# Kernel optimization log

Measured on AMD Instinct MI355X. Metric: run time of the kernel, lower is better.

The kernel has to match this reference:

```python
import jax, jax.numpy as jnp
import numpy as np

TEMPERATURE = 0.07
EPS = 1e-8  # torch cosine_similarity clamps the norm product at eps


def setup_inputs() -> dict:
    key = jax.random.key(0)
    k1, k2 = jax.random.split(key)
    B, D = 8192, 256
    u = jax.random.normal(k1, (B, D), dtype=jnp.float32)
    v = jax.random.normal(k2, (B, D), dtype=jnp.float32)
    return {"u": u, "v": v}


def _cos_sim_matrix(a, b):
    # pairwise cosine similarity: (a . b) / max(|a||b|, eps)
    dots = a @ b.T                                   # [B, B]
    an = jnp.linalg.norm(a, axis=-1)                 # [B]
    bn = jnp.linalg.norm(b, axis=-1)                 # [B]
    denom = jnp.maximum(an[:, None] * bn[None, :], EPS)
    return dots / denom


def reference(u, v):
    B = u.shape[0]
    sim_uv = _cos_sim_matrix(u, v) / TEMPERATURE     # [B, B]
    sim_uu = _cos_sim_matrix(u, u) / TEMPERATURE     # [B, B]
    eye = jnp.eye(B, dtype=bool)
    pos_loss = jnp.diagonal(sim_uv)                  # [B]
    neg_inf = jnp.array(-jnp.inf, dtype=sim_uv.dtype)
    # off-diagonal entries of both matrices, concatenated per row (2B-2 valid each)
    negative_sim = jnp.concatenate(
        [jnp.where(eye, neg_inf, sim_uv), jnp.where(eye, neg_inf, sim_uu)], axis=1
    )                                                # [B, 2B]
    neg_loss = jax.nn.logsumexp(negative_sim, axis=-1)  # [B]
    return (-pos_loss + neg_loss).mean()
```

## Files before the change

kernel.cpp:

```cpp
#include <hip/hip_runtime.h>
#include <hip/hip_bf16.h>
#include <stdint.h>

#define NB 8192
#define ND 256
#define NW 16384
#define BM 128
#define BN 64
#define NSTRIP 4
#define STRIPW 4096
#define NPANEL (STRIPW / BN)
#define SQRT_SCALE 4.53981596f
#define LN2F 0.69314718f

typedef __bf16 bf16x8 __attribute__((ext_vector_type(8)));
typedef float floatx4 __attribute__((ext_vector_type(4)));

__device__ __forceinline__ void gload_lds16(const void* g, void* l) {
    __builtin_amdgcn_global_load_lds(
        (const __attribute__((address_space(1))) unsigned int*)g,
        (__attribute__((address_space(3))) unsigned int*)l,
        16, 0, 0);
}

__device__ __forceinline__ float fexp2(float x) {
    return __builtin_amdgcn_exp2f(x);
}

__global__ __launch_bounds__(512) void prep_kernel(
    const float* __restrict__ u, const float* __restrict__ v,
    __hip_bfloat16* __restrict__ W, float* __restrict__ out)
{
    const int t    = threadIdx.x;
    if (blockIdx.x == 0 && t == 0) out[0] = 0.f;
    const int row  = blockIdx.x * 8 + (t >> 6);
    const int lane = t & 63;
    const float* src = (row < NB) ? (v + (size_t)row * ND)
                                  : (u + (size_t)(row - NB) * ND);
    float4 x = ((const float4*)src)[lane];
    float ss = x.x * x.x + x.y * x.y + x.z * x.z + x.w * x.w;
#pragma unroll
    for (int off = 1; off < 64; off <<= 1) ss += __shfl_xor(ss, off, 64);
    const float sc = rsqrtf(ss) * SQRT_SCALE;
    ushort4 o;
    __hip_bfloat16 h;
    h = __float2bfloat16(x.x * sc); o.x = *(const unsigned short*)&h;
    h = __float2bfloat16(x.y * sc); o.y = *(const unsigned short*)&h;
    h = __float2bfloat16(x.z * sc); o.z = *(const unsigned short*)&h;
    h = __float2bfloat16(x.w * sc); o.w = *(const unsigned short*)&h;
    ((ushort4*)(W + (size_t)row * ND))[lane] = o;
}

__global__ __launch_bounds__(512, 2) void dcl_main(
    const __hip_bfloat16* __restrict__ W,
    float* __restrict__ partial,
    float* __restrict__ pos)
{
    const int b  = blockIdx.x;
    const int s  = (b >> 1) & 3;
    const int rt = ((b >> 3) << 1) | (b & 1);
    const int rb = rt * BM;

    const __hip_bfloat16* A = W + (size_t)NB * ND;

    __shared__ __align__(16) char lds[131072];

    const int tid  = threadIdx.x;
    const int wave = tid >> 6;
    const int lane = tid & 63;
    const int wm   = wave >> 2;
    const int wn   = wave & 3;
    const int quad = lane >> 4;
    const int tcol = lane & 15;
    const int rh   = lane >> 5;
    const int cl   = lane & 31;

    const int sbase = s * STRIPW;

#define WAITV(N) do {                                                        \
    asm volatile("s_waitcnt vmcnt(" #N ")" ::: "memory");                    \
    __builtin_amdgcn_sched_barrier(0);                                       \
} while (0)

#define STAGE(T) do {                                                        \
    char* dst_ = lds + ((T) & 3) * 32768 + wave * 4096;                      \
    const int cb_ = sbase + (T) * BN;                                        \
    _Pragma("unroll")                                                        \
    for (int i_ = 0; i_ < 4; i_++) {                                         \
        int rl_ = wave * 8 + i_ * 2 + rh;               \
        gload_lds16(W + (size_t)(cb_ + rl_) * ND + ((cl ^ (rl_ & 15)) << 3), \
                    dst_ + i_ * 1024);                                       \
    }                                                                        \
} while (0)

#define COMPUTE(T) do {                                                      \
    const char* sb_ = lds + ((T) & 3) * 32768;                               \
    _Pragma("unroll")                                                        \
    for (int mt_ = 0; mt_ < 4; mt_++) acc[mt_] = (floatx4){0.f,0.f,0.f,0.f}; \
    _Pragma("unroll")                                                        \
    for (int ks_ = 0; ks_ < 8; ks_++) {                                      \
        bf16x8 bb_ = *(const bf16x8*)(sb_ + (wn * 16 + tcol) * 512 +         \
                                      ((((ks_ * 4) + quad) ^ tcol) << 4));   \
        _Pragma("unroll")                                                    \
        for (int mt_ = 0; mt_ < 4; mt_++)                                    \
            acc[mt_] = __builtin_amdgcn_mfma_f32_16x16x32_bf16(              \
                af[mt_][ks_], bb_, acc[mt_], 0, 0, 0);                       \
    }                                                                        \
} while (0)

#define EPILOGUE(T) do {                                                     \
    const int cbE_ = sbase + (T) * BN;                                       \
    if (cbE_ != dp) {                                                        \
        _Pragma("unroll")                                                    \
        for (int mt_ = 0; mt_ < 4; mt_++)                                    \
            _Pragma("unroll")                                                \
            for (int rg_ = 0; rg_ < 4; rg_++)                                \
                rsum[mt_][rg_] += fexp2(acc[mt_][rg_]);                      \
    } else {                                                                 \
        _Pragma("unroll")                                                    \
        for (int mt_ = 0; mt_ < 4; mt_++)                                    \
            _Pragma("unroll")                                                \
            for (int rg_ = 0; rg_ < 4; rg_++) {                              \
                int rl_ = mt_ * 16 + quad * 4 + rg_;                         \
                bool sel_ = (rl_ == wn * 16 + tcol);                         \
                float sc_ = acc[mt_][rg_];                                   \
                if (sel_) posv = sc_;                                        \
                rsum[mt_][rg_] += sel_ ? 0.f : fexp2(sc_);                   \
            }                                                                \
    }                                                                        \
} while (0)

#define PANEL_BODY(T) do {                                                   \
    __builtin_amdgcn_s_setprio(1);                                           \
    COMPUTE(T);                                                              \
    EPILOGUE(T);                                                             \
    __builtin_amdgcn_s_setprio(0);                                           \
} while (0)

    bf16x8 af[4][8];
#pragma unroll
    for (int mt = 0; mt < 4; mt++) {
        const __hip_bfloat16* ar =
            A + (size_t)(rb + wm * 64 + mt * 16 + tcol) * ND + quad * 8;
#pragma unroll
        for (int ks = 0; ks < 8; ks++)
            af[mt][ks] = *(const bf16x8*)(ar + ks * 32);
    }

    STAGE(0); STAGE(1); STAGE(2);

    const bool isuv = (s < 2);
    int dp = rb + wm * 64 + (isuv ? 0 : NB);
    const bool dvalid = ((dp >> 12) == s);
    if (!dvalid) dp = 0x40000000;

    float rsum[4][4];
#pragma unroll
    for (int mt = 0; mt < 4; mt++)
#pragma unroll
        for (int rg = 0; rg < 4; rg++) rsum[mt][rg] = 0.f;

    float posv = 0.f;
    floatx4 acc[4];

#pragma unroll 1
    for (int t = 0; t < NPANEL - 3; t++) {
        WAITV(8);
        __builtin_amdgcn_s_barrier();
        STAGE(t + 3);
        __builtin_amdgcn_sched_barrier(0);
        PANEL_BODY(t);
    }
    WAITV(8);  __builtin_amdgcn_s_barrier(); PANEL_BODY(61);
    WAITV(4);  __builtin_amdgcn_s_barrier(); PANEL_BODY(62);
    WAITV(0);  __builtin_amdgcn_s_barrier(); PANEL_BODY(63);

#undef WAITV
#undef STAGE
#undef COMPUTE
#undef EPILOGUE
#undef PANEL_BODY

    if (isuv && dvalid && (tcol >> 2) == quad)
        pos[rb + wm * 64 + wn * 16 + tcol] = posv * LN2F;

    __syncthreads();

#pragma unroll
    for (int mt = 0; mt < 4; mt++)
#pragma unroll
        for (int reg = 0; reg < 4; reg++) {
            float vsum = rsum[mt][reg];
            vsum += __shfl_xor(vsum, 1, 64);
            vsum += __shfl_xor(vsum, 2, 64);
            vsum += __shfl_xor(vsum, 4, 64);
            vsum += __shfl_xor(vsum, 8, 64);
            if (tcol == 0) {
                int lrow = wm * 64 + mt * 16 + quad * 4 + reg;
                ((float*)lds)[wn * 128 + lrow] = vsum;
            }
        }
    __syncthreads();
    if (tid < BM) {
        const float* lf = (const float*)lds;
        float t = lf[tid] + lf[128 + tid] + lf[256 + tid] + lf[384 + tid];
        partial[(size_t)s * NB + rb + tid] = t;
    }
}

__global__ __launch_bounds__(256) void finalize_kernel(
    const float* __restrict__ partial, const float* __restrict__ pos,
    float* __restrict__ out)
{
    const int i = blockIdx.x * 256 + threadIdx.x;
    float tot = partial[i] + partial[NB + i] + partial[2 * NB + i]
              + partial[3 * NB + i];
    float sv = logf(tot) - pos[i];
#pragma unroll
    for (int off = 32; off > 0; off >>= 1) sv += __shfl_down(sv, off, 64);
    __shared__ float wsum[4];
    const int t = threadIdx.x;
    if ((t & 63) == 0) wsum[t >> 6] = sv;
    __syncthreads();
    if (t == 0) {
        float blk = (wsum[0] + wsum[1]) + (wsum[2] + wsum[3]);
        atomicAdd(out, blk / (float)NB);
    }
}

extern "C" void kernel_launch(void* const* d_in, const int* in_sizes, int n_in,
                              void* d_out, int out_size, void* d_ws, size_t ws_size,
                              hipStream_t stream) {
    const float* u = (const float*)d_in[0];
    const float* v = (const float*)d_in[1];
    float* out = (float*)d_out;

    char* ws = (char*)d_ws;
    __hip_bfloat16* W = (__hip_bfloat16*)ws;
    float* partial = (float*)(ws + (size_t)NW * ND * sizeof(__hip_bfloat16));
    float* pos     = partial + NSTRIP * NB;

    prep_kernel<<<NW / 8, 512, 0, stream>>>(u, v, W, out);
    dcl_main<<<256, 512, 0, stream>>>(W, partial, pos);
    finalize_kernel<<<NB / 256, 256, 0, stream>>>(partial, pos, out);
}
```

Measured before the change: 135.6 us.

## Remap waves to 16-row strips and overlap exp epilogue with next panel's MFMAs

Each wave now owns 16 A rows across all 64 panel columns instead of a 64x16 tile, so A fragments shrink from 4x8 to 8 registers while B fragments are re-read from LDS per n-tile. Accumulators are double-buffered so the exp2/row-sum of the previous panel is interleaved with the current panel's MFMAs using sched_group_barrier, and the diagonal term is subtracted afterwards in a fixup. The final reduction drops the LDS cross-wave combine and writes per-row partials directly from shuffles. It costs four times as many LDS B reads per wave and relies on the -1e38 initial accumulators to make the first exp2 contribute zero.

```diff
diff --git a/kernel.cpp b/kernel.cpp
--- a/kernel.cpp
+++ b/kernel.cpp
@@ -68,8 +68,6 @@
     const int tid  = threadIdx.x;
     const int wave = tid >> 6;
     const int lane = tid & 63;
-    const int wm   = wave >> 2;
-    const int wn   = wave & 3;
     const int quad = lane >> 4;
     const int tcol = lane & 15;
     const int rh   = lane >> 5;
@@ -93,118 +91,116 @@
     }                                                                        \
 } while (0)
 
-#define COMPUTE(T) do {                                                      \
+#define COMPUTE_EPI(T, ACCC, ACCP) do {                                      \
     const char* sb_ = lds + ((T) & 3) * 32768;                               \
     _Pragma("unroll")                                                        \
-    for (int mt_ = 0; mt_ < 4; mt_++) acc[mt_] = (floatx4){0.f,0.f,0.f,0.f}; \
+    for (int nt_ = 0; nt_ < 4; nt_++) ACCC[nt_] = (floatx4){0.f,0.f,0.f,0.f};\
     _Pragma("unroll")                                                        \
     for (int ks_ = 0; ks_ < 8; ks_++) {                                      \
-        bf16x8 bb_ = *(const bf16x8*)(sb_ + (wn * 16 + tcol) * 512 +         \
-                                      ((((ks_ * 4) + quad) ^ tcol) << 4));   \
         _Pragma("unroll")                                                    \
-        for (int mt_ = 0; mt_ < 4; mt_++)                                    \
-            acc[mt_] = __builtin_amdgcn_mfma_f32_16x16x32_bf16(              \
-                af[mt_][ks_], bb_, acc[mt_], 0, 0, 0);                       \
-    }                                                                        \
-} while (0)
-
-#define EPILOGUE(T) do {                                                     \
-    const int cbE_ = sbase + (T) * BN;                                       \
-    if (cbE_ != dp) {                                                        \
+        for (int nt_ = 0; nt_ < 4; nt_++) {                                  \
+            bf16x8 bb_ = *(const bf16x8*)(sb_ + (nt_ * 16 + tcol) * 512 +    \
+                                          ((((ks_ * 4) + quad) ^ tcol) << 4));\
+            ACCC[nt_] = __builtin_amdgcn_mfma_f32_16x16x32_bf16(             \
+                af[ks_], bb_, ACCC[nt_], 0, 0, 0);                           \
+        }                                                                    \
+    }                                                                        \
+    _Pragma("unroll")                                                        \
+    for (int nt_ = 0; nt_ < 4; nt_++)                                        \
         _Pragma("unroll")                                                    \
-        for (int mt_ = 0; mt_ < 4; mt_++)                                    \
-            _Pragma("unroll")                                                \
-            for (int rg_ = 0; rg_ < 4; rg_++)                                \
-                rsum[mt_][rg_] += fexp2(acc[mt_][rg_]);                      \
-    } else {                                                                 \
+        for (int rg_ = 0; rg_ < 4; rg_++)                                    \
+            rsum[rg_] += fexp2(ACCP[nt_][rg_]);                              \
+    __builtin_amdgcn_sched_group_barrier(0x100, 4, 0);       \
+    _Pragma("unroll")                                                        \
+    for (int g_ = 0; g_ < 8; g_++) {                                         \
+        __builtin_amdgcn_sched_group_barrier(0x008, 4, 0);      \
+        __builtin_amdgcn_sched_group_barrier(0x002, 8, 0);      \
+        if (g_ < 7) __builtin_amdgcn_sched_group_barrier(0x100, 4, 0);       \
+    }                                                                        \
+} while (0)
+
+#define FIXUP(ACCP, T) do {                                                  \
+    if (sbase + (T) * BN == dpp) {                                           \
         _Pragma("unroll")                                                    \
-        for (int mt_ = 0; mt_ < 4; mt_++)                                    \
+        for (int nt_ = 0; nt_ < 4; nt_++)                                    \
             _Pragma("unroll")                                                \
             for (int rg_ = 0; rg_ < 4; rg_++) {                              \
-                int rl_ = mt_ * 16 + quad * 4 + rg_;                         \
-                bool sel_ = (rl_ == wn * 16 + tcol);                         \
-                float sc_ = acc[mt_][rg_];                                   \
-                if (sel_) posv = sc_;                                        \
-                rsum[mt_][rg_] += sel_ ? 0.f : fexp2(sc_);                   \
+                bool sel_ = (nt_ == dnt) && (tcol == quad * 4 + rg_);        \
+                float sc_ = ACCP[nt_][rg_];                                  \
+                if (sel_) { posv = sc_; rsum[rg_] -= fexp2(sc_); }           \
             }                                                                \
     }                                                                        \
 } while (0)
 
-#define PANEL_BODY(T) do {                                                   \
+#define PHASE(T, ACCC, ACCP, NWAIT, DOSTAGE) do {                            \
+    WAITV(NWAIT);                                                            \
+    __builtin_amdgcn_s_barrier();                                            \
+    if (DOSTAGE) STAGE((T) + 3);                                             \
+    __builtin_amdgcn_sched_barrier(0);                                       \
     __builtin_amdgcn_s_setprio(1);                                           \
-    COMPUTE(T);                                                              \
-    EPILOGUE(T);                                                             \
+    COMPUTE_EPI(T, ACCC, ACCP);                                              \
     __builtin_amdgcn_s_setprio(0);                                           \
-} while (0)
-
-    bf16x8 af[4][8];
-#pragma unroll
-    for (int mt = 0; mt < 4; mt++) {
+    FIXUP(ACCP, (T) - 1);                                                    \
+} while (0)
+
+    bf16x8 af[8];
+    {
         const __hip_bfloat16* ar =
-            A + (size_t)(rb + wm * 64 + mt * 16 + tcol) * ND + quad * 8;
+            A + (size_t)(rb + wave * 16 + tcol) * ND + quad * 8;
 #pragma unroll
         for (int ks = 0; ks < 8; ks++)
-            af[mt][ks] = *(const bf16x8*)(ar + ks * 32);
+            af[ks] = *(const bf16x8*)(ar + ks * 32);
     }
 
     STAGE(0); STAGE(1); STAGE(2);
 
     const bool isuv = (s < 2);
-    int dp = rb + wm * 64 + (isuv ? 0 : NB);
+    const int  dp = rb + wave * 16 + (isuv ? 0 : NB);
     const bool dvalid = ((dp >> 12) == s);
-    if (!dvalid) dp = 0x40000000;
-
-    float rsum[4][4];
-#pragma unroll
-    for (int mt = 0; mt < 4; mt++)
-#pragma unroll
-        for (int rg = 0; rg < 4; rg++) rsum[mt][rg] = 0.f;
-
+    const int  dpp = dvalid ? (dp & ~63) : 0x40000000;
+    const int  dnt = (dp >> 4) & 3;
+
+    float rsum[4] = {0.f, 0.f, 0.f, 0.f};
     float posv = 0.f;
-    floatx4 acc[4];
+    floatx4 accA[4], accB[4];
+#pragma unroll
+    for (int nt = 0; nt < 4; nt++)
+        accB[nt] = (floatx4){-1e38f, -1e38f, -1e38f, -1e38f};
 
 #pragma unroll 1
-    for (int t = 0; t < NPANEL - 3; t++) {
-        WAITV(8);
-        __builtin_amdgcn_s_barrier();
-        STAGE(t + 3);
-        __builtin_amdgcn_sched_barrier(0);
-        PANEL_BODY(t);
-    }
-    WAITV(8);  __builtin_amdgcn_s_barrier(); PANEL_BODY(61);
-    WAITV(4);  __builtin_amdgcn_s_barrier(); PANEL_BODY(62);
-    WAITV(0);  __builtin_amdgcn_s_barrier(); PANEL_BODY(63);
+    for (int t = 0; t < NPANEL - 4; t += 2) {
+        PHASE(t,     accA, accB, 8, 1);
+        PHASE(t + 1, accB, accA, 8, 1);
+    }
+    PHASE(60, accA, accB, 8, 1);
+    PHASE(61, accB, accA, 8, 0);
+    PHASE(62, accA, accB, 4, 0);
+    PHASE(63, accB, accA, 0, 0);
+#pragma unroll
+    for (int nt = 0; nt < 4; nt++)
+#pragma unroll
+        for (int rg = 0; rg < 4; rg++)
+            rsum[rg] += fexp2(accB[nt][rg]);
+    FIXUP(accB, 63);
 
 #undef WAITV
 #undef STAGE
-#undef COMPUTE
-#undef EPILOGUE
-#undef PANEL_BODY
+#undef COMPUTE_EPI
+#undef FIXUP
+#undef PHASE
 
     if (isuv && dvalid && (tcol >> 2) == quad)
-        pos[rb + wm * 64 + wn * 16 + tcol] = posv * LN2F;
-
-    __syncthreads();
-
-#pragma unroll
-    for (int mt = 0; mt < 4; mt++)
-#pragma unroll
-        for (int reg = 0; reg < 4; reg++) {
-            float vsum = rsum[mt][reg];
-            vsum += __shfl_xor(vsum, 1, 64);
-            vsum += __shfl_xor(vsum, 2, 64);
-            vsum += __shfl_xor(vsum, 4, 64);
-            vsum += __shfl_xor(vsum, 8, 64);
-            if (tcol == 0) {
-                int lrow = wm * 64 + mt * 16 + quad * 4 + reg;
-                ((float*)lds)[wn * 128 + lrow] = vsum;
-            }
-        }
-    __syncthreads();
-    if (tid < BM) {
-        const float* lf = (const float*)lds;
-        float t = lf[tid] + lf[128 + tid] + lf[256 + tid] + lf[384 + tid];
-        partial[(size_t)s * NB + rb + tid] = t;
+        pos[rb + wave * 16 + quad * 4 + (tcol & 3)] = posv * LN2F;
+
+#pragma unroll
+    for (int rg = 0; rg < 4; rg++) {
+        float v = rsum[rg];
+        v += __shfl_xor(v, 1, 16);
+        v += __shfl_xor(v, 2, 16);
+        v += __shfl_xor(v, 4, 16);
+        v += __shfl_xor(v, 8, 16);
+        if (tcol == 0)
+            partial[(size_t)s * NB + rb + wave * 16 + quad * 4 + rg] = v;
     }
 }
 
```

Measured after the change: 140.4 us. 1.04x slower.
